# Kernel optimization log

Measured on AMD Instinct MI355X. Metric: run time of the kernel, lower is better.

## Reference

```python
import jax, jax.numpy as jnp
import numpy as np

EPS = 1e-5
HID = 32
FUSED = 33 * 33 * 33  # 35937


def _subnet(x, gamma, beta, W1, b1, W2, b2, W3, b3):
    # BatchNorm1d in training mode: batch mean / biased variance
    mu = jnp.mean(x, axis=0)
    var = jnp.mean((x - mu) ** 2, axis=0)
    xn = (x - mu) / jnp.sqrt(var + EPS) * gamma + beta
    h = jax.nn.relu(xn @ W1 + b1)
    h = jax.nn.relu(h @ W2 + b2)
    return jax.nn.relu(h @ W3 + b3)


def _subnet_params(key, in_dim):
    ks = jax.random.split(key, 6)
    s_in = 1.0 / np.sqrt(in_dim)
    s_h = 1.0 / np.sqrt(HID)
    return dict(
        gamma=jnp.ones((in_dim,), jnp.float32),
        beta=jnp.zeros((in_dim,), jnp.float32),
        W1=jax.random.uniform(ks[0], (in_dim, HID), jnp.float32, -s_in, s_in),
        b1=jax.random.uniform(ks[1], (HID,), jnp.float32, -s_in, s_in),
        W2=jax.random.uniform(ks[2], (HID, HID), jnp.float32, -s_h, s_h),
        b2=jax.random.uniform(ks[3], (HID,), jnp.float32, -s_h, s_h),
        W3=jax.random.uniform(ks[4], (HID, HID), jnp.float32, -s_h, s_h),
        b3=jax.random.uniform(ks[5], (HID,), jnp.float32, -s_h, s_h),
    )


def setup_inputs() -> dict:
    key = jax.random.key(0)
    ks = jax.random.split(key, 10)
    B = 8192
    inp = {
        'US_x': jax.random.normal(ks[0], (B, 1024), jnp.float32),
        'CDFI_x': jax.random.normal(ks[1], (B, 1024), jnp.float32),
        'marker_x': jax.random.normal(ks[2], (B, 10), jnp.float32),
    }
    for pref, k, d in (('us', ks[3], 1024), ('cd', ks[4], 1024), ('mk', ks[5], 10)):
        for n, v in _subnet_params(k, d).items():
            inp[f'{pref}_{n}'] = v
    s1 = 1.0 / np.sqrt(FUSED)
    s2 = 1.0 / np.sqrt(33)
    inp['Wf1'] = jax.random.uniform(ks[6], (FUSED, 33), jnp.float32, -s1, s1)
    inp['bf1'] = jax.random.uniform(ks[7], (33,), jnp.float32, -s1, s1)
    inp['Wf2'] = jax.random.uniform(ks[8], (33, 5), jnp.float32, -s2, s2)
    inp['bf2'] = jax.random.uniform(ks[9], (5,), jnp.float32, -s2, s2)
    return inp


def reference(US_x, CDFI_x, marker_x,
              us_gamma, us_beta, us_W1, us_b1, us_W2, us_b2, us_W3, us_b3,
              cd_gamma, cd_beta, cd_W1, cd_b1, cd_W2, cd_b2, cd_W3, cd_b3,
              mk_gamma, mk_beta, mk_W1, mk_b1, mk_W2, mk_b2, mk_W3, mk_b3,
              Wf1, bf1, Wf2, bf2):
    B = US_x.shape[0]
    us_h = _subnet(US_x, us_gamma, us_beta, us_W1, us_b1, us_W2, us_b2, us_W3, us_b3)
    cd_h = _subnet(CDFI_x, cd_gamma, cd_beta, cd_W1, cd_b1, cd_W2, cd_b2, cd_W3, cd_b3)
    mk_h = _subnet(marker_x, mk_gamma, mk_beta, mk_W1, mk_b1, mk_W2, mk_b2, mk_W3, mk_b3)
    ones = jnp.ones((B, 1), jnp.float32)
    us1 = jnp.concatenate([ones, us_h], axis=1)   # [B,33]
    cd1 = jnp.concatenate([ones, cd_h], axis=1)   # [B,33]
    mk1 = jnp.concatenate([ones, mk_h], axis=1)   # [B,33]
    # fused[b,k,j,i] = mk1[b,k] * cd1[b,j] * us1[b,i]; flattened row-major
    fused = jnp.einsum('bk,bj,bi->bkji', mk1, cd1, us1).reshape(B, FUSED)
    h = jax.nn.relu(fused @ Wf1 + bf1)
    return jax.nn.sigmoid(h @ Wf2 + bf2)
```

## Files before the change

### kernel.cpp

```cpp
#include <hip/hip_runtime.h>
#include <hip/hip_bf16.h>
#include <math.h>

typedef __hip_bfloat16 bf16;
typedef __attribute__((ext_vector_type(4))) float f32x4;
typedef __attribute__((ext_vector_type(8))) short s16x8;

#define NB 8192
#define KP 1120
#define NP 1152

struct SubP {
    const float* x; const float* gamma; const float* beta;
    const float* W1; const float* b1; const float* W2; const float* b2;
    const float* W3; const float* b3;
    float* sum; float* sumsq; float* a; float* b1p; float* hout;
    int F;
};
struct SubP3 { SubP s[3]; };

__global__ void __launch_bounds__(256) stats3_kernel(SubP3 P) {
    const SubP p = P.s[blockIdx.z];
    int t = threadIdx.x;
    int row0 = blockIdx.x * 64;
    if (p.F == 1024) {
        f32x4 s = {0.f, 0.f, 0.f, 0.f}, s2 = {0.f, 0.f, 0.f, 0.f};
        const float* xp = p.x + (size_t)row0 * 1024 + t * 4;
        #pragma unroll 8
        for (int r = 0; r < 64; r++) {
            f32x4 v = *(const f32x4*)(xp + (size_t)r * 1024);
            s += v; s2 += v * v;
        }
        int f = t * 4;
        #pragma unroll
        for (int e = 0; e < 4; e++) {
            atomicAdd(&p.sum[f + e], s[e]);
            atomicAdd(&p.sumsq[f + e], s2[e]);
        }
    } else {
        __shared__ float ls[16], ls2[16];
        if (t < 16) { ls[t] = 0.f; ls2[t] = 0.f; }
        __syncthreads();
        int F = p.F;
        for (int idx = t; idx < 64 * F; idx += 256) {
            float v = p.x[(size_t)row0 * F + idx];
            int f = idx % 10;
            atomicAdd(&ls[f], v);
            atomicAdd(&ls2[f], v * v);
        }
        __syncthreads();
        if (t < F) { atomicAdd(&p.sum[t], ls[t]); atomicAdd(&p.sumsq[t], ls2[t]); }
    }
}

__global__ void prep3_kernel(SubP3 P) {
    const SubP p = P.s[blockIdx.y];
    int f0 = blockIdx.x * 32;
    if (f0 >= p.F) return;
    int t = threadIdx.x;
    __shared__ float c_sh[32];
    __shared__ float red[8][33];
    int fc = p.F - f0; if (fc > 32) fc = 32;
    if (t < 32) {
        float c = 0.f;
        if (t < fc) {
            int f = f0 + t;
            float mu  = p.sum[f]   * (1.f / 8192.f);
            float var = p.sumsq[f] * (1.f / 8192.f) - mu * mu;
            float a = p.gamma[f] * rsqrtf(var + 1e-5f);
            p.a[f] = a;
            c = p.beta[f] - mu * a;
        }
        c_sh[t] = c;
    }
    __syncthreads();
    int h = t & 31, g = t >> 5;
    float s = 0.f;
    for (int fi = g; fi < fc; fi += 8)
        s += c_sh[fi] * p.W1[(size_t)(f0 + fi) * 32 + h];
    red[g][h] = s;
    __syncthreads();
    if (t < 32) {
        float tot = 0.f;
        #pragma unroll
        for (int gg = 0; gg < 8; gg++) tot += red[gg][t];
        atomicAdd(&p.b1p[t], tot);
    }
}

__global__ void __launch_bounds__(256) subnet3_kernel(SubP3 P) {
    const SubP p = P.s[blockIdx.y];
    const int F = p.F;
    __shared__ float smem[8832];
    float* Red = smem;
    float* H1  = smem + 3456;
    float* W23 = smem + 4608;
    float* H2  = smem;

    int t = threadIdx.x;
    int row0 = blockIdx.x * 32;
    int kg = t >> 6;
    int lane = t & 63;
    int hg = lane & 7, h0 = hg * 4;
    int rg = (lane >> 3) & 3;
    int ks = lane >> 5;

    float acc[4][8] = {};

    if (F == 1024) {
        float* Xt = smem;
        float* Wt = smem + 4224;
        int xr = t >> 3, xc = (t & 7) * 16;
        int wk = t >> 1, wh = (t & 1) * 16;
        const float* xbase = p.x + (size_t)row0 * 1024;
        f32x4 xp[4], wp[4]; float av;
        #pragma unroll
        for (int i = 0; i < 4; i++) xp[i] = *(const f32x4*)&xbase[(size_t)xr * 1024 + xc + i * 4];
        #pragma unroll
        for (int i = 0; i < 4; i++) wp[i] = *(const f32x4*)&p.W1[(size_t)wk * 32 + wh + i * 4];
        av = p.a[wk];
        int kb = (kg * 2 + ks) * 16;
        for (int c = 0; c < 8; c++) {
            __syncthreads();
            #pragma unroll
            for (int i = 0; i < 4; i++) *(f32x4*)&Xt[xr * 132 + xc + i * 4] = xp[i];
            #pragma unroll
            for (int i = 0; i < 4; i++) *(f32x4*)&Wt[wk * 36 + wh + i * 4] = wp[i] * av;
            if (c < 7) {
                int k0 = (c + 1) * 128;
                #pragma unroll
                for (int i = 0; i < 4; i++) xp[i] = *(const f32x4*)&xbase[(size_t)xr * 1024 + k0 + xc + i * 4];
                #pragma unroll
                for (int i = 0; i < 4; i++) wp[i] = *(const f32x4*)&p.W1[(size_t)(k0 + wk) * 32 + wh + i * 4];
                av = p.a[k0 + wk];
            }
            __syncthreads();
            #pragma unroll
            for (int s = 0; s < 4; s++) {
                int kk = kb + s * 4;
                f32x4 wv[4], xv[8];
                #pragma unroll
                for (int j = 0; j < 4; j++)  wv[j]  = *(const f32x4*)&Wt[(kk + j) * 36 + h0];
                #pragma unroll
                for (int ri = 0; ri < 8; ri++) xv[ri] = *(const f32x4*)&Xt[(rg + 4 * ri) * 132 + kk];
                #pragma unroll
                for (int j = 0; j < 4; j++)
                    #pragma unroll
                    for (int hi = 0; hi < 4; hi++) {
                        float w = wv[j][hi];
                        #pragma unroll
                        for (int ri = 0; ri < 8; ri++)
                            acc[hi][ri] = fmaf(w, xv[ri][j], acc[hi][ri]);
                    }
            }
        }
    } else {
        float* Xt = smem;
        float* Wt = smem + 2176;
        int kbase = (kg * 2 + ks) * 8;
        for (int k0 = 0; k0 < F; k0 += 64) {
            int kc = F - k0; if (kc > 64) kc = 64;
            int kcp = (kc + 3) & ~3;
            __syncthreads();
            for (int idx = t; idx < 32 * kcp; idx += 256) {
                int r = idx / kcp, kk = idx - r * kcp;
                Xt[r * 68 + kk] = (kk < kc) ? p.x[(size_t)(row0 + r) * F + k0 + kk] : 0.f;
            }
            for (int idx = t; idx < kcp * 32; idx += 256) {
                int kk = idx >> 5, hh = idx & 31;
                Wt[kk * 36 + hh] = (kk < kc) ? p.a[k0 + kk] * p.W1[(size_t)(k0 + kk) * 32 + hh] : 0.f;
            }
            __syncthreads();
            #pragma unroll
            for (int s = 0; s < 2; s++) {
                int kk = kbase + s * 4;
                if (kk < kcp) {
                    f32x4 wv[4], xv[8];
                    #pragma unroll
                    for (int j = 0; j < 4; j++)  wv[j]  = *(const f32x4*)&Wt[(kk + j) * 36 + h0];
                    #pragma unroll
                    for (int ri = 0; ri < 8; ri++) xv[ri] = *(const f32x4*)&Xt[(rg + 4 * ri) * 68 + kk];
                    #pragma unroll
                    for (int j = 0; j < 4; j++)
                        #pragma unroll
                        for (int hi = 0; hi < 4; hi++) {
                            float w = wv[j][hi];
                            #pragma unroll
                            for (int ri = 0; ri < 8; ri++)
                                acc[hi][ri] = fmaf(w, xv[ri][j], acc[hi][ri]);
                        }
                }
            }
        }
    }
    #pragma unroll
    for (int hi = 0; hi < 4; hi++)
        #pragma unroll
        for (int ri = 0; ri < 8; ri++)
            acc[hi][ri] += __shfl_xor(acc[hi][ri], 32);
    __syncthreads();
    if (kg > 0 && ks == 0) {
        #pragma unroll
        for (int ri = 0; ri < 8; ri++) {
            int r = rg + 4 * ri;
            f32x4 v = {acc[0][ri], acc[1][ri], acc[2][ri], acc[3][ri]};
            *(f32x4*)&Red[(kg - 1) * 1152 + r * 36 + h0] = v;
        }
    }
    for (int idx = t; idx < 1024; idx += 256) W23[(idx >> 5) * 33 + (idx & 31)] = p.W2[idx];
    __syncthreads();
    if (kg == 0 && ks == 0) {
        f32x4 b;
        #pragma unroll
        for (int hi = 0; hi < 4; hi++) b[hi] = p.b1[h0 + hi] + p.b1p[h0 + hi];
        #pragma unroll
        for (int ri = 0; ri < 8; ri++) {
            int r = rg + 4 * ri;
            f32x4 v = {acc[0][ri], acc[1][ri], acc[2][ri], acc[3][ri]};
            #pragma unroll
            for (int pp = 0; pp < 3; pp++)
                v += *(const f32x4*)&Red[pp * 1152 + r * 36 + h0];
            v += b;
            #pragma unroll
            for (int hi = 0; hi < 4; hi++)
                H1[r * 36 + h0 + hi] = fmaxf(v[hi], 0.f);
        }
    }
    __syncthreads();
    int h = t & 31, rq = t >> 5;
    {
        float a2[4] = {};
        for (int q = 0; q < 32; q++) {
            float w = W23[q * 33 + h];
            #pragma unroll
            for (int i = 0; i < 4; i++) a2[i] += H1[(rq * 4 + i) * 36 + q] * w;
        }
        float bv = p.b2[h];
        #pragma unroll
        for (int i = 0; i < 4; i++) H2[(rq * 4 + i) * 36 + h] = fmaxf(a2[i] + bv, 0.f);
    }
    __syncthreads();
    for (int idx = t; idx < 1024; idx += 256) W23[(idx >> 5) * 33 + (idx & 31)] = p.W3[idx];
    __syncthreads();
    {
        float a3[4] = {};
        for (int q = 0; q < 32; q++) {
            float w = W23[q * 33 + h];
            #pragma unroll
            for (int i = 0; i < 4; i++) a3[i] += H2[(rq * 4 + i) * 36 + q] * w;
        }
        float bv = p.b3[h];
        #pragma unroll
        for (int i = 0; i < 4; i++)
            p.hout[(size_t)(row0 + rq * 4 + i) * 32 + h] = fmaxf(a3[i] + bv, 0.f);
    }
}

__global__ void build_both(const float* __restrict__ mk_h, const float* __restrict__ us_h,
                           bf16* __restrict__ p1,
                           const float* __restrict__ Wf1, bf16* __restrict__ W2t) {
    int blk = blockIdx.x;
    int t = threadIdx.x;
    if (blk < NB) {
        int b = blk;
        __shared__ float mk1[33], us1[33];
        if (t == 0) { mk1[0] = 1.f; us1[0] = 1.f; }
        if (t < 32) mk1[t + 1] = mk_h[(size_t)b * 32 + t];
        else if (t < 64) us1[t - 31] = us_h[(size_t)b * 32 + (t - 32)];
        __syncthreads();
        if (t < 140) {
            int base = t * 8;
            s16x8 v;
            #pragma unroll
            for (int e = 0; e < 8; e++) {
                int idx = base + e;
                float val = 0.f;
                if (idx < 1089) {
                    int k = idx / 33, i = idx - k * 33;
                    val = mk1[k] * us1[i];
                }
                __hip_bfloat16 hb = __float2bfloat16(val);
                v[e] = *(short*)&hb;
            }
            *(s16x8*)(p1 + (size_t)b * KP + base) = v;
        }
    } else {
        int kj = blk - NB;
        int k = kj / 33, j = kj - k * 33;
        __shared__ float tile[1089];
        const float* src = Wf1 + (size_t)k * 35937 + (size_t)j * 1089;
        for (int idx = t; idx < 1089; idx += 192) tile[idx] = src[idx];
        __syncthreads();
        for (int idx = t; idx < 1089; idx += 192) {
            int o = idx / 33, i = idx - o * 33;
            W2t[(size_t)(j * 33 + o) * KP + k * 33 + i] = __float2bfloat16(tile[i * 33 + o]);
        }
        if (k == 0) {
            bf16 z = __float2bfloat16(0.f);
            for (int idx = t; idx < 33 * 31; idx += 192) {
                int o = idx / 31, kkp = 1089 + idx - o * 31;
                W2t[(size_t)(j * 33 + o) * KP + kkp] = z;
            }
        }
    }
}

__global__ void __launch_bounds__(256) gemm_kernel(const bf16* __restrict__ A,
                                                   const bf16* __restrict__ Bt,
                                                   bf16* __restrict__ S) {
    __shared__ __align__(16) bf16 As[128 * 32];
    __shared__ __align__(16) bf16 Bs[128 * 32];
    int t = threadIdx.x;
    int m0 = blockIdx.x * 128;
    int n0 = blockIdx.y * 128;
    int wave = t >> 6, lane = t & 63;
    int wm = (wave & 1) * 64, wn = (wave >> 1) * 64;
    int fr = lane & 15;
    int kg = (lane >> 4) * 8;

    int lr = lane >> 2;
    int lk = (lane & 3) * 8;
    const bf16* Ag = A  + (size_t)(m0 + wave * 32 + lr) * KP + lk;
    const bf16* Bg = Bt + (size_t)(n0 + wave * 32 + lr) * KP + lk;
    bf16* AsW = As + wave * 32 * 32;
    bf16* BsW = Bs + wave * 32 * 32;

    f32x4 acc[4][4] = {};

    for (int k0 = 0; k0 < KP; k0 += 32) {
        __syncthreads();
        __builtin_amdgcn_global_load_lds(
            (const __attribute__((address_space(1))) void*)(Ag + k0),
            (__attribute__((address_space(3))) void*)(AsW), 16, 0, 0);
        __builtin_amdgcn_global_load_lds(
            (const __attribute__((address_space(1))) void*)(Ag + k0 + 16 * KP),
            (__attribute__((address_space(3))) void*)(AsW + 16 * 32), 16, 0, 0);
        __builtin_amdgcn_global_load_lds(
            (const __attribute__((address_space(1))) void*)(Bg + k0),
            (__attribute__((address_space(3))) void*)(BsW), 16, 0, 0);
        __builtin_amdgcn_global_load_lds(
            (const __attribute__((address_space(1))) void*)(Bg + k0 + 16 * KP),
            (__attribute__((address_space(3))) void*)(BsW + 16 * 32), 16, 0, 0);
        __syncthreads();
        s16x8 bfr[4];
        #pragma unroll
        for (int nt = 0; nt < 4; nt++)
            bfr[nt] = *(const s16x8*)(Bs + (wn + nt * 16 + fr) * 32 + kg);
        #pragma unroll
        for (int mt = 0; mt < 4; mt++) {
            s16x8 af = *(const s16x8*)(As + (wm + mt * 16 + fr) * 32 + kg);
            #pragma unroll
            for (int nt = 0; nt < 4; nt++)
                acc[mt][nt] = __builtin_amdgcn_mfma_f32_16x16x32_bf16(af, bfr[nt], acc[mt][nt], 0, 0, 0);
        }
    }
    int col = lane & 15, rowg = (lane >> 4) * 4;
    #pragma unroll
    for (int mt = 0; mt < 4; mt++)
        #pragma unroll
        for (int nt = 0; nt < 4; nt++)
            #pragma unroll
            for (int r = 0; r < 4; r++) {
                int gr = m0 + wm + mt * 16 + rowg + r;
                int gc = n0 + wn + nt * 16 + col;
                S[(size_t)gr * NP + gc] = __float2bfloat16(acc[mt][nt][r]);
            }
}

__global__ void __launch_bounds__(256) epilogue_kernel(const bf16* __restrict__ S,
                                const float* __restrict__ cd_h,
                                const float* __restrict__ bf1, const float* __restrict__ Wf2,
                                const float* __restrict__ bf2, float* __restrict__ out) {
    int w = threadIdx.x >> 6;
    int lane = threadIdx.x & 63;
    int b = blockIdx.x * 4 + w;
    __shared__ __align__(16) unsigned short Sl[4][1152];
    __shared__ float cdsh[4][33];
    __shared__ float hsh[4][40];
    const bf16* Srow = S + (size_t)b * NP;
    #pragma unroll
    for (int pass = 0; pass < 3; pass++) {
        int idx = lane + pass * 64;
        if (idx < 144)
            *(s16x8*)&Sl[w][idx * 8] = *(const s16x8*)(Srow + idx * 8);
    }
    if (lane == 0) cdsh[w][0] = 1.f;
    if (lane < 32) cdsh[w][lane + 1] = cd_h[(size_t)b * 32 + lane];
    __syncthreads();
    if (lane < 33) {
        float acc = bf1[lane];
        #pragma unroll 3
        for (int j = 0; j < 33; j++) {
            unsigned short sv = Sl[w][j * 33 + lane];
            acc += cdsh[w][j] * __bfloat162float(*(bf16*)&sv);
        }
        hsh[w][lane] = fmaxf(acc, 0.f);
    }
    __syncthreads();
    if (lane < 5) {
        float o = bf2[lane];
        for (int q = 0; q < 33; q++) o += hsh[w][q] * Wf2[q * 5 + lane];
        out[(size_t)b * 5 + lane] = 1.f / (1.f + expf(-o));
    }
}

extern "C" void kernel_launch(void* const* d_in, const int* in_sizes, int n_in,
                              void* d_out, int out_size, void* d_ws, size_t ws_size,
                              hipStream_t stream) {
    const float* US_x     = (const float*)d_in[0];
    const float* CDFI_x   = (const float*)d_in[1];
    const float* marker_x = (const float*)d_in[2];
    const float* Wf1      = (const float*)d_in[27];
    const float* bf1      = (const float*)d_in[28];
    const float* Wf2      = (const float*)d_in[29];
    const float* bf2      = (const float*)d_in[30];
    float* out = (float*)d_out;

    char* ws = (char*)d_ws;
    size_t off = 0;
    auto alloc = [&](size_t bytes) -> void* {
        void* p = ws + off;
        off = (off + bytes + 255) & ~(size_t)255;
        return p;
    };

    float* stat_big = (float*)alloc(3 * 2176 * sizeof(float));
    float* a_buf[3], *h_buf[3];
    for (int i = 0; i < 3; i++) {
        a_buf[i] = (float*)alloc(1024 * 4);
        h_buf[i] = (float*)alloc((size_t)NB * 32 * 4);
    }
    bf16*  p1   = (bf16*)alloc((size_t)NB * KP * 2);
    bf16*  W2t  = (bf16*)alloc((size_t)NP * KP * 2);
    bf16*  S    = (bf16*)alloc((size_t)NB * NP * 2);

    SubP3 P;
    const float* xs[3] = {US_x, CDFI_x, marker_x};
    int Fs[3] = {1024, 1024, 10};
    for (int i = 0; i < 3; i++) {
        int base = 3 + i * 8;
        P.s[i].x     = xs[i];
        P.s[i].gamma = (const float*)d_in[base + 0];
        P.s[i].beta  = (const float*)d_in[base + 1];
        P.s[i].W1    = (const float*)d_in[base + 2];
        P.s[i].b1    = (const float*)d_in[base + 3];
        P.s[i].W2    = (const float*)d_in[base + 4];
        P.s[i].b2    = (const float*)d_in[base + 5];
        P.s[i].W3    = (const float*)d_in[base + 6];
        P.s[i].b3    = (const float*)d_in[base + 7];
        P.s[i].sum   = stat_big + i * 2176;
        P.s[i].sumsq = stat_big + i * 2176 + 1024;
        P.s[i].b1p   = stat_big + i * 2176 + 2048;
        P.s[i].a     = a_buf[i];
        P.s[i].hout  = h_buf[i];
        P.s[i].F     = Fs[i];
    }

    float* us_h = h_buf[0];
    float* cd_h = h_buf[1];
    float* mk_h = h_buf[2];

    hipMemsetAsync(stat_big, 0, 3 * 2176 * sizeof(float), stream);

    stats3_kernel<<<dim3(128, 1, 3), 256, 0, stream>>>(P);
    prep3_kernel<<<dim3(32, 3), 256, 0, stream>>>(P);
    subnet3_kernel<<<dim3(256, 3), 256, 0, stream>>>(P);

    build_both<<<NB + 1089, 192, 0, stream>>>(mk_h, us_h, p1, Wf1, W2t);

    gemm_kernel<<<dim3(NB / 128, NP / 128), 256, 0, stream>>>(p1, W2t, S);

    epilogue_kernel<<<NB / 4, 256, 0, stream>>>(S, cd_h, bf1, Wf2, bf2, out);
}
```

Measured before the change: 258.2 us.

## Double-buffer GEMM LDS tiles with K=64 steps and XOR-swizzled layout

Pads K from 1120 to 1152 so the reduction runs in 18 steps of 64. The GEMM now double-buffers its LDS tiles, issuing the next stage's global-to-LDS loads before computing on the current buffer, which leaves one barrier per step instead of two. An XOR swizzle on the 16-byte chunk index is meant to avoid LDS bank conflicts on the fragment reads. In exchange it doubles LDS use per block, which may reduce occupancy, and adds a little padded work in K.

```diff
diff --git a/kernel.cpp b/kernel.cpp
--- a/kernel.cpp
+++ b/kernel.cpp
@@ -7,8 +7,9 @@
 typedef __attribute__((ext_vector_type(8))) short s16x8;
 
 #define NB 8192
-#define KP 1120
+#define KP 1152
 #define NP 1152
+#define NK 18
 
 struct SubP {
     const float* x; const float* gamma; const float* beta;
@@ -268,7 +269,7 @@
         if (t < 32) mk1[t + 1] = mk_h[(size_t)b * 32 + t];
         else if (t < 64) us1[t - 31] = us_h[(size_t)b * 32 + (t - 32)];
         __syncthreads();
-        if (t < 140) {
+        if (t < 144) {
             int base = t * 8;
             s16x8 v;
             #pragma unroll
@@ -297,8 +298,8 @@
         }
         if (k == 0) {
             bf16 z = __float2bfloat16(0.f);
-            for (int idx = t; idx < 33 * 31; idx += 192) {
-                int o = idx / 31, kkp = 1089 + idx - o * 31;
+            for (int idx = t; idx < 33 * 63; idx += 192) {
+                int o = idx / 63, kkp = 1089 + idx - o * 63;
                 W2t[(size_t)(j * 33 + o) * KP + kkp] = z;
             }
         }
@@ -308,51 +309,64 @@
 __global__ void __launch_bounds__(256) gemm_kernel(const bf16* __restrict__ A,
                                                    const bf16* __restrict__ Bt,
                                                    bf16* __restrict__ S) {
-    __shared__ __align__(16) bf16 As[128 * 32];
-    __shared__ __align__(16) bf16 Bs[128 * 32];
+    __shared__ __align__(16) bf16 As[2][128 * 64];
+    __shared__ __align__(16) bf16 Bs[2][128 * 64];
     int t = threadIdx.x;
     int m0 = blockIdx.x * 128;
     int n0 = blockIdx.y * 128;
     int wave = t >> 6, lane = t & 63;
     int wm = (wave & 1) * 64, wn = (wave >> 1) * 64;
     int fr = lane & 15;
-    int kg = (lane >> 4) * 8;
-
-    int lr = lane >> 2;
-    int lk = (lane & 3) * 8;
-    const bf16* Ag = A  + (size_t)(m0 + wave * 32 + lr) * KP + lk;
-    const bf16* Bg = Bt + (size_t)(n0 + wave * 32 + lr) * KP + lk;
-    bf16* AsW = As + wave * 32 * 32;
-    bf16* BsW = Bs + wave * 32 * 32;
+    int q  = lane >> 4;
+
+    int lr8 = lane >> 3;
+    int slt = (lane & 7) ^ lr8;
+    const bf16* Ag = A  + (size_t)(m0 + wave * 32 + lr8) * KP + slt * 8;
+    const bf16* Bg = Bt + (size_t)(n0 + wave * 32 + lr8) * KP + slt * 8;
 
     f32x4 acc[4][4] = {};
 
-    for (int k0 = 0; k0 < KP; k0 += 32) {
+    auto stage = [&](int buf, int k0) {
+        bf16* Ad = &As[buf][wave * 2048];
+        bf16* Bd = &Bs[buf][wave * 2048];
+        #pragma unroll
+        for (int i = 0; i < 4; i++) {
+            __builtin_amdgcn_global_load_lds(
+                (const __attribute__((address_space(1))) void*)(Ag + k0 + (size_t)i * 8 * KP),
+                (__attribute__((address_space(3))) void*)(Ad + i * 512), 16, 0, 0);
+            __builtin_amdgcn_global_load_lds(
+                (const __attribute__((address_space(1))) void*)(Bg + k0 + (size_t)i * 8 * KP),
+                (__attribute__((address_space(3))) void*)(Bd + i * 512), 16, 0, 0);
+        }
+    };
+
+    stage(0, 0);
+    __syncthreads();
+    int cur = 0;
+    for (int ks = 0; ks < NK; ks++) {
+        if (ks < NK - 1) stage(cur ^ 1, (ks + 1) * 64);
+        const bf16* Ab = &As[cur][0];
+        const bf16* Bb = &Bs[cur][0];
+        #pragma unroll
+        for (int kk = 0; kk < 2; kk++) {
+            int xs = kk * 4 + q;
+            s16x8 bfr[4];
+            #pragma unroll
+            for (int nt = 0; nt < 4; nt++) {
+                int row = wn + nt * 16 + fr;
+                bfr[nt] = *(const s16x8*)(Bb + row * 64 + ((xs ^ (fr & 7)) * 8));
+            }
+            #pragma unroll
+            for (int mt = 0; mt < 4; mt++) {
+                int row = wm + mt * 16 + fr;
+                s16x8 af = *(const s16x8*)(Ab + row * 64 + ((xs ^ (fr & 7)) * 8));
+                #pragma unroll
+                for (int nt = 0; nt < 4; nt++)
+                    acc[mt][nt] = __builtin_amdgcn_mfma_f32_16x16x32_bf16(af, bfr[nt], acc[mt][nt], 0, 0, 0);
+            }
+        }
         __syncthreads();
-        __builtin_amdgcn_global_load_lds(
-            (const __attribute__((address_space(1))) void*)(Ag + k0),
-            (__attribute__((address_space(3))) void*)(AsW), 16, 0, 0);
-        __builtin_amdgcn_global_load_lds(
-            (const __attribute__((address_space(1))) void*)(Ag + k0 + 16 * KP),
-            (__attribute__((address_space(3))) void*)(AsW + 16 * 32), 16, 0, 0);
-        __builtin_amdgcn_global_load_lds(
-            (const __attribute__((address_space(1))) void*)(Bg + k0),
-            (__attribute__((address_space(3))) void*)(BsW), 16, 0, 0);
-        __builtin_amdgcn_global_load_lds(
-            (const __attribute__((address_space(1))) void*)(Bg + k0 + 16 * KP),
-            (__attribute__((address_space(3))) void*)(BsW + 16 * 32), 16, 0, 0);
-        __syncthreads();
-        s16x8 bfr[4];
-        #pragma unroll
-        for (int nt = 0; nt < 4; nt++)
-            bfr[nt] = *(const s16x8*)(Bs + (wn + nt * 16 + fr) * 32 + kg);
-        #pragma unroll
-        for (int mt = 0; mt < 4; mt++) {
-            s16x8 af = *(const s16x8*)(As + (wm + mt * 16 + fr) * 32 + kg);
-            #pragma unroll
-            for (int nt = 0; nt < 4; nt++)
-                acc[mt][nt] = __builtin_amdgcn_mfma_f32_16x16x32_bf16(af, bfr[nt], acc[mt][nt], 0, 0, 0);
-        }
+        cur ^= 1;
     }
     int col = lane & 15, rowg = (lane >> 4) * 4;
     #pragma unroll
```

New measurement: 266.8 us. 3.3% more time.

## Pre-swizzle GEMM operands into MFMA fragment layout and load directly to registers

Applied to the files above, without the earlier changes.

The build kernel now writes the activation and weight operands in a blocked layout that matches the MFMA 16x16x32 fragment order, and K is padded to 1152. The GEMM kernel then drops LDS staging and barriers: each wave loads its fragments straight from global memory into registers with coalesced 16-byte loads, double-buffered across K steps. This removes the LDS round-trip and the syncthreads, but fragments shared between waves are now fetched separately by each wave, relying on L2/cache, and the padding adds a little extra K work.

```diff
diff --git a/kernel.cpp b/kernel.cpp
--- a/kernel.cpp
+++ b/kernel.cpp
@@ -7,8 +7,10 @@
 typedef __attribute__((ext_vector_type(8))) short s16x8;
 
 #define NB 8192
-#define KP 1120
+#define KP 1152
 #define NP 1152
+#define NK 36
+
 
 struct SubP {
     const float* x; const float* gamma; const float* beta;
@@ -268,7 +270,7 @@
         if (t < 32) mk1[t + 1] = mk_h[(size_t)b * 32 + t];
         else if (t < 64) us1[t - 31] = us_h[(size_t)b * 32 + (t - 32)];
         __syncthreads();
-        if (t < 140) {
+        if (t < 144) {
             int base = t * 8;
             s16x8 v;
             #pragma unroll
@@ -282,7 +284,10 @@
                 __hip_bfloat16 hb = __float2bfloat16(val);
                 v[e] = *(short*)&hb;
             }
-            *(s16x8*)(p1 + (size_t)b * KP + base) = v;
+            int mb = b >> 7, rr = b & 127;
+            int h = rr >> 6, mt = (rr >> 4) & 3, fr = rr & 15;
+            size_t fo = ((size_t)(mb * 36 + (t >> 2)) * 8 + h * 4 + mt) * 64 + (t & 3) * 16 + fr;
+            *(s16x8*)(p1 + fo * 8) = v;
         }
     } else {
         int kj = blk - NB;
@@ -293,68 +298,74 @@
         __syncthreads();
         for (int idx = t; idx < 1089; idx += 192) {
             int o = idx / 33, i = idx - o * 33;
-            W2t[(size_t)(j * 33 + o) * KP + k * 33 + i] = __float2bfloat16(tile[i * 33 + o]);
+            int R = j * 33 + o;
+            int C = k * 33 + i;
+            int nb = R >> 7, rr = R & 127;
+            int hb = rr >> 6, nt = (rr >> 4) & 3, fr = rr & 15;
+            int kss = C >> 5, q = (C >> 3) & 3, e = C & 7;
+            size_t fo = ((size_t)(nb * 36 + kss) * 8 + hb * 4 + nt) * 64 + q * 16 + fr;
+            W2t[fo * 8 + e] = __float2bfloat16(tile[i * 33 + o]);
         }
         if (k == 0) {
             bf16 z = __float2bfloat16(0.f);
-            for (int idx = t; idx < 33 * 31; idx += 192) {
-                int o = idx / 31, kkp = 1089 + idx - o * 31;
-                W2t[(size_t)(j * 33 + o) * KP + kkp] = z;
-            }
-        }
-    }
-}
-
-__global__ void __launch_bounds__(256) gemm_kernel(const bf16* __restrict__ A,
-                                                   const bf16* __restrict__ Bt,
+            for (int idx = t; idx < 33 * 63; idx += 192) {
+                int o = idx / 63, C = 1089 + idx - o * 63;
+                int R = j * 33 + o;
+                int nb = R >> 7, rr = R & 127;
+                int hb = rr >> 6, nt = (rr >> 4) & 3, fr = rr & 15;
+                int kss = C >> 5, q = (C >> 3) & 3, e = C & 7;
+                size_t fo = ((size_t)(nb * 36 + kss) * 8 + hb * 4 + nt) * 64 + q * 16 + fr;
+                W2t[fo * 8 + e] = z;
+            }
+        }
+    }
+}
+
+__global__ void __launch_bounds__(256) gemm_kernel(const bf16* __restrict__ pA,
+                                                   const bf16* __restrict__ pB,
                                                    bf16* __restrict__ S) {
-    __shared__ __align__(16) bf16 As[128 * 32];
-    __shared__ __align__(16) bf16 Bs[128 * 32];
     int t = threadIdx.x;
-    int m0 = blockIdx.x * 128;
-    int n0 = blockIdx.y * 128;
+    int mb = blockIdx.x, nb = blockIdx.y;
     int wave = t >> 6, lane = t & 63;
-    int wm = (wave & 1) * 64, wn = (wave >> 1) * 64;
-    int fr = lane & 15;
-    int kg = (lane >> 4) * 8;
-
-    int lr = lane >> 2;
-    int lk = (lane & 3) * 8;
-    const bf16* Ag = A  + (size_t)(m0 + wave * 32 + lr) * KP + lk;
-    const bf16* Bg = Bt + (size_t)(n0 + wave * 32 + lr) * KP + lk;
-    bf16* AsW = As + wave * 32 * 32;
-    bf16* BsW = Bs + wave * 32 * 32;
+    int h = wave & 1, hb = wave >> 1;
+    int wm = h * 64, wn = hb * 64;
+
+    const s16x8* Ap = (const s16x8*)pA + ((size_t)mb * 36 * 8 + h * 4) * 64 + lane;
+    const s16x8* Bp = (const s16x8*)pB + ((size_t)nb * 36 * 8 + hb * 4) * 64 + lane;
 
     f32x4 acc[4][4] = {};
-
-    for (int k0 = 0; k0 < KP; k0 += 32) {
-        __syncthreads();
-        __builtin_amdgcn_global_load_lds(
-            (const __attribute__((address_space(1))) void*)(Ag + k0),
-            (__attribute__((address_space(3))) void*)(AsW), 16, 0, 0);
-        __builtin_amdgcn_global_load_lds(
-            (const __attribute__((address_space(1))) void*)(Ag + k0 + 16 * KP),
-            (__attribute__((address_space(3))) void*)(AsW + 16 * 32), 16, 0, 0);
-        __builtin_amdgcn_global_load_lds(
-            (const __attribute__((address_space(1))) void*)(Bg + k0),
-            (__attribute__((address_space(3))) void*)(BsW), 16, 0, 0);
-        __builtin_amdgcn_global_load_lds(
-            (const __attribute__((address_space(1))) void*)(Bg + k0 + 16 * KP),
-            (__attribute__((address_space(3))) void*)(BsW + 16 * 32), 16, 0, 0);
-        __syncthreads();
-        s16x8 bfr[4];
-        #pragma unroll
-        for (int nt = 0; nt < 4; nt++)
-            bfr[nt] = *(const s16x8*)(Bs + (wn + nt * 16 + fr) * 32 + kg);
-        #pragma unroll
-        for (int mt = 0; mt < 4; mt++) {
-            s16x8 af = *(const s16x8*)(As + (wm + mt * 16 + fr) * 32 + kg);
+    s16x8 a0[4], b0[4], a1[4], b1[4];
+
+    #pragma unroll
+    for (int mt = 0; mt < 4; mt++) a0[mt] = Ap[mt * 64];
+    #pragma unroll
+    for (int nt = 0; nt < 4; nt++) b0[nt] = Bp[nt * 64];
+
+    for (int ks = 0; ks < NK; ks += 2) {
+        #pragma unroll
+        for (int mt = 0; mt < 4; mt++) a1[mt] = Ap[(ks + 1) * 512 + mt * 64];
+        #pragma unroll
+        for (int nt = 0; nt < 4; nt++) b1[nt] = Bp[(ks + 1) * 512 + nt * 64];
+        #pragma unroll
+        for (int mt = 0; mt < 4; mt++)
             #pragma unroll
             for (int nt = 0; nt < 4; nt++)
-                acc[mt][nt] = __builtin_amdgcn_mfma_f32_16x16x32_bf16(af, bfr[nt], acc[mt][nt], 0, 0, 0);
-        }
-    }
+                acc[mt][nt] = __builtin_amdgcn_mfma_f32_16x16x32_bf16(a0[mt], b0[nt], acc[mt][nt], 0, 0, 0);
+        if (ks + 2 < NK) {
+            #pragma unroll
+            for (int mt = 0; mt < 4; mt++) a0[mt] = Ap[(ks + 2) * 512 + mt * 64];
+            #pragma unroll
+            for (int nt = 0; nt < 4; nt++) b0[nt] = Bp[(ks + 2) * 512 + nt * 64];
+        }
+        #pragma unroll
+        for (int mt = 0; mt < 4; mt++)
+            #pragma unroll
+            for (int nt = 0; nt < 4; nt++)
+                acc[mt][nt] = __builtin_amdgcn_mfma_f32_16x16x32_bf16(a1[mt], b1[nt], acc[mt][nt], 0, 0, 0);
+    }
+
     int col = lane & 15, rowg = (lane >> 4) * 4;
+    int m0 = mb * 128, n0 = nb * 128;
     #pragma unroll
     for (int mt = 0; mt < 4; mt++)
         #pragma unroll
```

New measurement: 276.9 us. 1.07x slower.
